# Performance work log

Hardware: AMD Instinct MI355X
Metric: run time of the kernel (lower is better)

## Reference

```python
import jax, jax.numpy as jnp
import numpy as np

N_NODES = 100000
N_EDGES = 3200000
D_IN = 512
D_HID = 512
D_OUT = 256


def setup_inputs() -> dict:
    key = jax.random.key(0)
    ks = jax.random.split(key, 7)
    x = jax.random.normal(ks[0], (N_NODES, D_IN), dtype=jnp.float32)
    edge_row = jax.random.randint(ks[1], (N_EDGES,), 0, N_NODES, dtype=jnp.int32)
    edge_col = jax.random.randint(ks[2], (N_EDGES,), 0, N_NODES, dtype=jnp.int32)
    edge_val = jax.random.uniform(ks[3], (N_EDGES,), dtype=jnp.float32)
    # Kaiming-uniform-ish init like torch Linear (bias=False)
    W0 = jax.random.normal(ks[4], (D_HID, D_IN), dtype=jnp.float32) / np.sqrt(D_IN)
    W1 = jax.random.normal(ks[5], (D_HID, D_HID), dtype=jnp.float32) / np.sqrt(D_HID)
    W2 = jax.random.normal(ks[6], (D_OUT, D_HID), dtype=jnp.float32) / np.sqrt(D_HID)
    return {"x": x, "edge_row": edge_row, "edge_col": edge_col,
            "edge_val": edge_val, "W0": W0, "W1": W1, "W2": W2}


def reference(x, edge_row, edge_col, edge_val, W0, W1, W2):
    # Layer 0: Linear (no bias) then sparse adjacency matmul (COO segment-sum)
    h = jnp.einsum('nd,hd->nh', x, W0)                      # [N, D_HID]
    msgs = edge_val[:, None] * h[edge_col]                  # gather source features [E, D_HID]
    h = jax.ops.segment_sum(msgs, edge_row, num_segments=N_NODES)  # scatter-add to rows
    h = jax.nn.relu(h)                                      # dropout p=0.0 -> identity
    # Middle layer (num_hidden=3 -> one middle layer): Linear + ReLU
    h = jax.nn.relu(jnp.einsum('nd,hd->nh', h, W1))
    # Final layer: Linear only
    out = jnp.einsum('nd,od->no', h, W2)                    # [N, D_OUT]
    return out
```

## Files before the change

kernel.cpp:

```cpp
#include <hip/hip_runtime.h>

typedef short  s16x8 __attribute__((ext_vector_type(8)));
typedef __bf16 bf16x8 __attribute__((ext_vector_type(8)));
typedef float  f32x4 __attribute__((ext_vector_type(4)));

#define AS1(p) ((const __attribute__((address_space(1))) void*)(p))
#define AS3(p) ((__attribute__((address_space(3))) void*)(p))

__global__ void cast_f32_bf16(const float* __restrict__ in, __bf16* __restrict__ out, int n8){
  int stride = gridDim.x * blockDim.x;
  for (int i = blockIdx.x * blockDim.x + threadIdx.x; i < n8; i += stride){
    const float4* p = (const float4*)in + 2*(size_t)i;
    float4 a = p[0], b = p[1];
    bf16x8 o;
    o[0]=(__bf16)a.x; o[1]=(__bf16)a.y; o[2]=(__bf16)a.z; o[3]=(__bf16)a.w;
    o[4]=(__bf16)b.x; o[5]=(__bf16)b.y; o[6]=(__bf16)b.z; o[7]=(__bf16)b.w;
    ((bf16x8*)out)[i] = o;
  }
}

__global__ void hist_rows(const int* __restrict__ rows, int* __restrict__ counts, int n){
  int stride = gridDim.x * blockDim.x;
  for (int i = blockIdx.x * blockDim.x + threadIdx.x; i < n; i += stride)
    atomicAdd(&counts[rows[i]], 1);
}

__global__ __launch_bounds__(1024) void scan_rows(const int* __restrict__ counts,
    int* __restrict__ row_ptr, int* __restrict__ cursor, int n){
  __shared__ int sb[1024];
  int t = threadIdx.x;
  int L = (n + 1023) / 1024;
  int lo = t * L, hi = lo + L; if (hi > n) hi = n; if (lo > n) lo = n;
  int sum = 0;
  for (int i = lo; i < hi; i++) sum += counts[i];
  sb[t] = sum;
  __syncthreads();
  for (int d = 1; d < 1024; d <<= 1){
    int v = (t >= d) ? sb[t - d] : 0;
    __syncthreads();
    sb[t] += v;
    __syncthreads();
  }
  int run = sb[t] - sum;
  for (int i = lo; i < hi; i++){
    row_ptr[i] = run; cursor[i] = run; run += counts[i];
  }
  if (t == 1023) row_ptr[n] = sb[1023];
}

__global__ void scatter_edges(const int* __restrict__ rows, const int* __restrict__ cols,
    const float* __restrict__ vals, int* __restrict__ cursor,
    int* __restrict__ ocol, float* __restrict__ oval, int n){
  int stride = gridDim.x * blockDim.x;
  for (int i = blockIdx.x * blockDim.x + threadIdx.x; i < n; i += stride){
    int r = rows[i];
    int p = atomicAdd(&cursor[r], 1);
    ocol[p] = cols[i];
    oval[p] = vals[i];
  }
}

__global__ __launch_bounds__(256) void spmm_relu(
    const int* __restrict__ rp, const int* __restrict__ cols, const float* __restrict__ vals,
    const __bf16* __restrict__ H, __bf16* __restrict__ O, int n){
  int w = (blockIdx.x * 256 + threadIdx.x) >> 6;
  int lane = threadIdx.x & 63;
  if (w >= n) return;
  int s = rp[w], e = rp[w + 1];
  float acc[8] = {0,0,0,0,0,0,0,0};
  for (int i = s; i < e; i++){
    int c = cols[i];
    float v = vals[i];
    s16x8 hv = *(const s16x8*)(H + (size_t)c * 512 + lane * 8);
    #pragma unroll
    for (int k = 0; k < 8; k++){
      unsigned u = ((unsigned)(unsigned short)hv[k]) << 16;
      acc[k] = fmaf(v, __builtin_bit_cast(float, u), acc[k]);
    }
  }
  s16x8 o;
  #pragma unroll
  for (int k = 0; k < 8; k++){
    float v = fmaxf(acc[k], 0.f);
    o[k] = __builtin_bit_cast(short, (__bf16)v);
  }
  *(s16x8*)(O + (size_t)w * 512 + lane * 8) = o;
}

template<int RELU, int OUT_BF16>
__global__ __launch_bounds__(256) void gemm_bt(
    const __bf16* __restrict__ A, const __bf16* __restrict__ B,
    void* __restrict__ C, int M, int N, int K){
  __shared__ __attribute__((aligned(16))) __bf16 As[128 * 64];
  __shared__ __attribute__((aligned(16))) __bf16 Bs[128 * 64];
  const int ntiles = N >> 7;
  const int tm = blockIdx.x / ntiles;
  const int tn = blockIdx.x % ntiles;
  const int row0 = tm << 7, col0 = tn << 7;
  const int tid = threadIdx.x;
  const int lane = tid & 63, wid = tid >> 6;
  const int wm = (wid >> 1) * 64, wn = (wid & 1) * 64;
  const int lr = lane & 15;
  const int lkb = ((lane >> 4) * 8) * 2;

  f32x4 acc[4][4] = {};

  for (int k0 = 0; k0 < K; k0 += 64){
    __syncthreads();
    #pragma unroll
    for (int i = 0; i < 4; i++){
      int bo = tid * 16 + i * 4096;
      int r  = bo >> 7;
      int cb = bo & 127;
      int ga = row0 + r; ga = ga < M ? ga : M - 1;
      __builtin_amdgcn_global_load_lds(AS1(A + (size_t)ga * K + k0 + (cb >> 1)),
                                       AS3((char*)As + (wid << 10) + i * 4096), 16, 0, 0);
      int gb = col0 + r;
      __builtin_amdgcn_global_load_lds(AS1(B + (size_t)gb * K + k0 + (cb >> 1)),
                                       AS3((char*)Bs + (wid << 10) + i * 4096), 16, 0, 0);
    }
    __syncthreads();
    #pragma unroll
    for (int kk = 0; kk < 2; kk++){
      s16x8 af[4], bfr[4];
      #pragma unroll
      for (int i = 0; i < 4; i++)
        af[i] = *(const s16x8*)((const char*)As + (wm + i * 16 + lr) * 128 + kk * 64 + lkb);
      #pragma unroll
      for (int j = 0; j < 4; j++)
        bfr[j] = *(const s16x8*)((const char*)Bs + (wn + j * 16 + lr) * 128 + kk * 64 + lkb);
      #pragma unroll
      for (int i = 0; i < 4; i++)
        #pragma unroll
        for (int j = 0; j < 4; j++)
          acc[i][j] = __builtin_amdgcn_mfma_f32_16x16x32_bf16(af[i], bfr[j], acc[i][j], 0, 0, 0);
    }
  }

  const int orow = (lane >> 4) * 4;
  #pragma unroll
  for (int i = 0; i < 4; i++){
    #pragma unroll
    for (int j = 0; j < 4; j++){
      int gc = col0 + wn + j * 16 + lr;
      #pragma unroll
      for (int r = 0; r < 4; r++){
        int gr = row0 + wm + i * 16 + orow + r;
        if (gr < M){
          float v = acc[i][j][r];
          if (RELU) v = fmaxf(v, 0.f);
          if (OUT_BF16) ((__bf16*)C)[(size_t)gr * N + gc] = (__bf16)v;
          else          ((float*)C)[(size_t)gr * N + gc] = v;
        }
      }
    }
  }
}

extern "C" void kernel_launch(void* const* d_in, const int* in_sizes, int n_in,
                              void* d_out, int out_size, void* d_ws, size_t ws_size,
                              hipStream_t stream){
  const float* x    = (const float*)d_in[0];
  const int*   erow = (const int*)d_in[1];
  const int*   ecol = (const int*)d_in[2];
  const float* eval = (const float*)d_in[3];
  const float* W0   = (const float*)d_in[4];
  const float* W1   = (const float*)d_in[5];
  const float* W2   = (const float*)d_in[6];

  const int DIN = 512, DH = 512, DO = 256;
  const int NN = in_sizes[0] / DIN;
  const int NE = in_sizes[1];

  size_t off = 0;
  auto carve = [&](size_t b) -> char* {
    char* p = (char*)d_ws + off; off += (b + 255) & ~(size_t)255; return p;
  };
  __bf16* bufA  = (__bf16*)carve((size_t)NN * DIN * 2);
  __bf16* bufB  = (__bf16*)carve((size_t)NN * DH * 2);
  __bf16* wW0   = (__bf16*)carve((size_t)DH * DIN * 2);
  __bf16* wW1   = (__bf16*)carve((size_t)DH * DH * 2);
  __bf16* wW2   = (__bf16*)carve((size_t)DO * DH * 2);
  int*   counts = (int*)carve((size_t)NN * 4);
  int*   rp     = (int*)carve(((size_t)NN + 1) * 4);
  int*   cursor = (int*)carve((size_t)NN * 4);
  int*   cs     = (int*)carve((size_t)NE * 4);
  float* vs     = (float*)carve((size_t)NE * 4);

  hipMemsetAsync(counts, 0, (size_t)NN * 4, stream);

  cast_f32_bf16<<<4096, 256, 0, stream>>>(x,  bufA, NN * DIN / 8);
  cast_f32_bf16<<<256,  256, 0, stream>>>(W0, wW0, DH * DIN / 8);
  cast_f32_bf16<<<256,  256, 0, stream>>>(W1, wW1, DH * DH / 8);
  cast_f32_bf16<<<128,  256, 0, stream>>>(W2, wW2, DO * DH / 8);

  hist_rows<<<2048, 256, 0, stream>>>(erow, counts, NE);
  scan_rows<<<1, 1024, 0, stream>>>(counts, rp, cursor, NN);
  scatter_edges<<<2048, 256, 0, stream>>>(erow, ecol, eval, cursor, cs, vs, NE);

  const int mt = (NN + 127) / 128;
  gemm_bt<0,1><<<dim3(mt * (DH / 128)), 256, 0, stream>>>(bufA, wW0, bufB, NN, DH, DIN);
  spmm_relu<<<(NN * 64 + 255) / 256, 256, 0, stream>>>(rp, cs, vs, bufB, bufA, NN);
  gemm_bt<1,1><<<dim3(mt * (DH / 128)), 256, 0, stream>>>(bufA, wW1, bufB, NN, DH, DH);
  gemm_bt<0,0><<<dim3(mt * (DO / 128)), 256, 0, stream>>>(bufB, wW2, d_out, NN, DO, DH);
}
```

Measured before the change: 1.627 ms.

## Parallelize row-pointer scan, pack edges as int2, batch SpMM edge loads via readlane

Replaces the single-block serial prefix scan with a three-phase multi-block scan (per-block int4 scan, block-sum scan, fixup). It also packs column and value into one int2 array, so the scatter does one write per edge and the SpMM does one read. In the SpMM, each wave loads up to 64 edges cooperatively, broadcasts them with readlane, and unrolls by four to keep several gathers in flight. The scan assumes NN is divisible by 4 and has at most 128 phase-A blocks, and rows with more than 64 edges fall back to a serial loop.

```diff
diff --git a/kernel.cpp b/kernel.cpp
--- a/kernel.cpp
+++ b/kernel.cpp
@@ -6,6 +6,11 @@
 
 #define AS1(p) ((const __attribute__((address_space(1))) void*)(p))
 #define AS3(p) ((__attribute__((address_space(3))) void*)(p))
+
+__device__ __forceinline__ float bf2f(short x){
+  unsigned u = ((unsigned)(unsigned short)x) << 16;
+  return __builtin_bit_cast(float, u);
+}
 
 __global__ void cast_f32_bf16(const float* __restrict__ in, __bf16* __restrict__ out, int n8){
   int stride = gridDim.x * blockDim.x;
@@ -25,59 +30,117 @@
     atomicAdd(&counts[rows[i]], 1);
 }
 
-__global__ __launch_bounds__(1024) void scan_rows(const int* __restrict__ counts,
-    int* __restrict__ row_ptr, int* __restrict__ cursor, int n){
-  __shared__ int sb[1024];
+__global__ __launch_bounds__(256) void scan_phaseA(const int* __restrict__ counts,
+    int* __restrict__ rp, int* __restrict__ bsum, int n4){
+  __shared__ int sb[256];
   int t = threadIdx.x;
-  int L = (n + 1023) / 1024;
-  int lo = t * L, hi = lo + L; if (hi > n) hi = n; if (lo > n) lo = n;
-  int sum = 0;
-  for (int i = lo; i < hi; i++) sum += counts[i];
-  sb[t] = sum;
-  __syncthreads();
-  for (int d = 1; d < 1024; d <<= 1){
+  int idx = blockIdx.x * 256 + t;
+  int4 c = make_int4(0,0,0,0);
+  if (idx < n4) c = ((const int4*)counts)[idx];
+  int s = c.x + c.y + c.z + c.w;
+  sb[t] = s; __syncthreads();
+  #pragma unroll
+  for (int d = 1; d < 256; d <<= 1){
     int v = (t >= d) ? sb[t - d] : 0;
     __syncthreads();
     sb[t] += v;
     __syncthreads();
   }
-  int run = sb[t] - sum;
-  for (int i = lo; i < hi; i++){
-    row_ptr[i] = run; cursor[i] = run; run += counts[i];
-  }
-  if (t == 1023) row_ptr[n] = sb[1023];
+  int ex = sb[t] - s;
+  if (idx < n4){
+    int4 o; o.x = ex; o.y = ex + c.x; o.z = o.y + c.y; o.w = o.z + c.z;
+    ((int4*)rp)[idx] = o;
+  }
+  if (t == 255) bsum[blockIdx.x] = sb[255];
+}
+
+__global__ __launch_bounds__(128) void scan_phaseB(int* __restrict__ bsum, int nb){
+  __shared__ int sb[128];
+  int t = threadIdx.x;
+  int v = (t < nb) ? bsum[t] : 0;
+  sb[t] = v; __syncthreads();
+  #pragma unroll
+  for (int d = 1; d < 128; d <<= 1){
+    int u = (t >= d) ? sb[t - d] : 0;
+    __syncthreads();
+    sb[t] += u;
+    __syncthreads();
+  }
+  if (t < nb) bsum[t] = sb[t] - v;
+}
+
+__global__ void scan_phaseC(const int* __restrict__ bsum, int* __restrict__ rp,
+    int* __restrict__ cursor, int n, int ne){
+  int i = blockIdx.x * 256 + threadIdx.x;
+  if (i < n){
+    int v = rp[i] + bsum[i >> 10];
+    rp[i] = v; cursor[i] = v;
+  }
+  if (i == 0) rp[n] = ne;
 }
 
 __global__ void scatter_edges(const int* __restrict__ rows, const int* __restrict__ cols,
     const float* __restrict__ vals, int* __restrict__ cursor,
-    int* __restrict__ ocol, float* __restrict__ oval, int n){
+    int2* __restrict__ ev, int n){
   int stride = gridDim.x * blockDim.x;
   for (int i = blockIdx.x * blockDim.x + threadIdx.x; i < n; i += stride){
     int r = rows[i];
     int p = atomicAdd(&cursor[r], 1);
-    ocol[p] = cols[i];
-    oval[p] = vals[i];
+    ev[p] = make_int2(cols[i], __float_as_int(vals[i]));
   }
 }
 
 __global__ __launch_bounds__(256) void spmm_relu(
-    const int* __restrict__ rp, const int* __restrict__ cols, const float* __restrict__ vals,
+    const int* __restrict__ rp, const int2* __restrict__ ev,
     const __bf16* __restrict__ H, __bf16* __restrict__ O, int n){
   int w = (blockIdx.x * 256 + threadIdx.x) >> 6;
   int lane = threadIdx.x & 63;
   if (w >= n) return;
   int s = rp[w], e = rp[w + 1];
+  int deg = e - s;
+  const __bf16* Hl = H + lane * 8;
   float acc[8] = {0,0,0,0,0,0,0,0};
-  for (int i = s; i < e; i++){
-    int c = cols[i];
-    float v = vals[i];
-    s16x8 hv = *(const s16x8*)(H + (size_t)c * 512 + lane * 8);
+
+  int2 cv = make_int2(0, 0);
+  if (lane < deg) cv = ev[s + lane];
+  int m = deg < 64 ? deg : 64;
+  int i = 0;
+  for (; i + 4 <= m; i += 4){
+    int c0 = __builtin_amdgcn_readlane(cv.x, i);
+    int c1 = __builtin_amdgcn_readlane(cv.x, i + 1);
+    int c2 = __builtin_amdgcn_readlane(cv.x, i + 2);
+    int c3 = __builtin_amdgcn_readlane(cv.x, i + 3);
+    float v0 = __builtin_bit_cast(float, __builtin_amdgcn_readlane(cv.y, i));
+    float v1 = __builtin_bit_cast(float, __builtin_amdgcn_readlane(cv.y, i + 1));
+    float v2 = __builtin_bit_cast(float, __builtin_amdgcn_readlane(cv.y, i + 2));
+    float v3 = __builtin_bit_cast(float, __builtin_amdgcn_readlane(cv.y, i + 3));
+    s16x8 h0 = *(const s16x8*)(Hl + (size_t)c0 * 512);
+    s16x8 h1 = *(const s16x8*)(Hl + (size_t)c1 * 512);
+    s16x8 h2 = *(const s16x8*)(Hl + (size_t)c2 * 512);
+    s16x8 h3 = *(const s16x8*)(Hl + (size_t)c3 * 512);
     #pragma unroll
     for (int k = 0; k < 8; k++){
-      unsigned u = ((unsigned)(unsigned short)hv[k]) << 16;
-      acc[k] = fmaf(v, __builtin_bit_cast(float, u), acc[k]);
-    }
-  }
+      acc[k] = fmaf(v0, bf2f(h0[k]), acc[k]);
+      acc[k] = fmaf(v1, bf2f(h1[k]), acc[k]);
+      acc[k] = fmaf(v2, bf2f(h2[k]), acc[k]);
+      acc[k] = fmaf(v3, bf2f(h3[k]), acc[k]);
+    }
+  }
+  for (; i < m; i++){
+    int c = __builtin_amdgcn_readlane(cv.x, i);
+    float v = __builtin_bit_cast(float, __builtin_amdgcn_readlane(cv.y, i));
+    s16x8 h0 = *(const s16x8*)(Hl + (size_t)c * 512);
+    #pragma unroll
+    for (int k = 0; k < 8; k++) acc[k] = fmaf(v, bf2f(h0[k]), acc[k]);
+  }
+  for (int j = s + 64; j < e; j++){
+    int2 p = ev[j];
+    float v = __builtin_bit_cast(float, p.y);
+    s16x8 h0 = *(const s16x8*)(Hl + (size_t)p.x * 512);
+    #pragma unroll
+    for (int k = 0; k < 8; k++) acc[k] = fmaf(v, bf2f(h0[k]), acc[k]);
+  }
+
   s16x8 o;
   #pragma unroll
   for (int k = 0; k < 8; k++){
@@ -184,8 +247,8 @@
   int*   counts = (int*)carve((size_t)NN * 4);
   int*   rp     = (int*)carve(((size_t)NN + 1) * 4);
   int*   cursor = (int*)carve((size_t)NN * 4);
-  int*   cs     = (int*)carve((size_t)NE * 4);
-  float* vs     = (float*)carve((size_t)NE * 4);
+  int*   bsum   = (int*)carve(4096);
+  int2*  ev     = (int2*)carve((size_t)NE * 8);
 
   hipMemsetAsync(counts, 0, (size_t)NN * 4, stream);
 
@@ -195,12 +258,16 @@
   cast_f32_bf16<<<128,  256, 0, stream>>>(W2, wW2, DO * DH / 8);
 
   hist_rows<<<2048, 256, 0, stream>>>(erow, counts, NE);
-  scan_rows<<<1, 1024, 0, stream>>>(counts, rp, cursor, NN);
-  scatter_edges<<<2048, 256, 0, stream>>>(erow, ecol, eval, cursor, cs, vs, NE);
+  const int n4 = NN / 4;
+  const int nblkA = (n4 + 255) / 256;
+  scan_phaseA<<<nblkA, 256, 0, stream>>>(counts, rp, bsum, n4);
+  scan_phaseB<<<1, 128, 0, stream>>>(bsum, nblkA);
+  scan_phaseC<<<(NN + 255) / 256, 256, 0, stream>>>(bsum, rp, cursor, NN, NE);
+  scatter_edges<<<2048, 256, 0, stream>>>(erow, ecol, eval, cursor, ev, NE);
 
   const int mt = (NN + 127) / 128;
   gemm_bt<0,1><<<dim3(mt * (DH / 128)), 256, 0, stream>>>(bufA, wW0, bufB, NN, DH, DIN);
-  spmm_relu<<<(NN * 64 + 255) / 256, 256, 0, stream>>>(rp, cs, vs, bufB, bufA, NN);
+  spmm_relu<<<(NN * 64 + 255) / 256, 256, 0, stream>>>(rp, ev, bufB, bufA, NN);
   gemm_bt<1,1><<<dim3(mt * (DH / 128)), 256, 0, stream>>>(bufA, wW1, bufB, NN, DH, DH);
   gemm_bt<0,0><<<dim3(mt * (DO / 128)), 256, 0, stream>>>(bufB, wW2, d_out, NN, DO, DH);
 }
```

New measurement: 1.450 ms. -10.9%, faster.
